# Kernel tuning notes

Hardware: AMD Instinct MI355X
Metric: run time of the kernel (lower is better)

Reference implementation:

```python
import jax, jax.numpy as jnp
import numpy as np

EPS = 1e-5
NUM_HEADS = 8
KEY_DEPTH = 128   # base_filters * key_expansion
VAL_DEPTH = 256   # base_filters * value_expansion
C_IN = 256


def conv1x1(x, w):
    # x: [N, Cin, L], w: [Cout, Cin] (1x1 conv, no bias)
    return jnp.einsum('oc,ncl->nol', w, x)


def group_norm1(x, w, b, eps=EPS):
    # torch GroupNorm(1, C) on [N, C, L]: normalize over (C, L) per sample,
    # per-channel affine.
    mu = jnp.mean(x, axis=(1, 2), keepdims=True)
    var = jnp.var(x, axis=(1, 2), keepdims=True)
    xn = (x - mu) * jax.lax.rsqrt(var + eps)
    return xn * w[None, :, None] + b[None, :, None]


def layer_norm_last2(x, eps=EPS):
    # freshly-constructed nn.LayerNorm([A, B]): weight=1, bias=0 -> pure norm
    mu = jnp.mean(x, axis=(-2, -1), keepdims=True)
    var = jnp.var(x, axis=(-2, -1), keepdims=True)
    return (x - mu) * jax.lax.rsqrt(var + eps)


def gelu(x):
    return jax.nn.gelu(x, approximate=False)  # torch F.gelu default (erf)


def setup_inputs() -> dict:
    key = jax.random.key(0)
    ks = jax.random.split(key, 16)
    N, L = 8, 1024
    qkv_out = 2 * KEY_DEPTH + VAL_DEPTH  # 512

    def w(k, shape, std=0.02):
        return jax.random.normal(k, shape, jnp.float32) * std

    def gw(k, c):
        return 1.0 + 0.1 * jax.random.normal(k, (c,), jnp.float32)

    return {
        'f': jax.random.normal(ks[0], (N, C_IN, L), jnp.float32),
        'w_z': w(ks[1], (C_IN, C_IN), np.sqrt(2.0 / C_IN)),
        'gz_w': gw(ks[2], C_IN), 'gz_b': w(ks[3], (C_IN,)),
        'w_qkv': w(ks[4], (qkv_out, C_IN), C_IN ** -0.5),
        'gq_w': gw(ks[5], qkv_out), 'gq_b': w(ks[6], (qkv_out,)),
        'w_out': w(ks[7], (C_IN, VAL_DEPTH), np.sqrt(2.0 / VAL_DEPTH)),
        'go_w': gw(ks[8], C_IN), 'go_b': w(ks[9], (C_IN,)),
        'w_ffn1': w(ks[10], (2 * C_IN, C_IN), np.sqrt(2.0 / C_IN)),
        'g1_w': gw(ks[11], 2 * C_IN), 'g1_b': w(ks[12], (2 * C_IN,)),
        'w_ffn2': w(ks[13], (C_IN, 2 * C_IN), np.sqrt(1.0 / C_IN)),
        'g2_w': gw(ks[14], C_IN), 'g2_b': w(ks[15], (C_IN,)),
    }


def reference(f, w_z, gz_w, gz_b, w_qkv, gq_w, gq_b, w_out, go_w, go_b,
              w_ffn1, g1_w, g1_b, w_ffn2, g2_w, g2_b):
    N, C, L = f.shape
    H = NUM_HEADS

    z = gelu(group_norm1(conv1x1(gelu(f), w_z), gz_w, gz_b))
    qkv = group_norm1(conv1x1(z, w_qkv), gq_w, gq_b)
    q, k, v = jnp.split(qkv, [KEY_DEPTH, 2 * KEY_DEPTH], axis=1)
    q = q.reshape(N, H, KEY_DEPTH // H, L)
    k = k.reshape(N, H, KEY_DEPTH // H, L)
    v = v.reshape(N, H, VAL_DEPTH // H, L)

    # [N, H, L, L] similarity, no scaling, then LayerNorm over full LxL map
    logits = jnp.einsum('nhcl,nhcm->nhlm', q, k)
    logits = layer_norm_last2(logits)

    # scatter-mask: diagonal -> -inf for every head
    eye = jnp.eye(L, dtype=bool)[None, None]  # [1,1,L,L]
    logits = jnp.where(eye, -jnp.inf, logits)

    attn = jax.nn.softmax(logits.astype(jnp.float32), axis=-1)
    attn = jnp.where(jnp.isnan(attn), 0.0, attn)

    out = jnp.einsum('nhlm,nhdm->nhdl', attn, v).reshape(N, VAL_DEPTH, L)
    out = gelu(layer_norm_last2(out))  # LayerNorm([C_v, L]), fresh params

    out = group_norm1(conv1x1(out, w_out), go_w, go_b)
    f = gelu(f + out)

    h = gelu(group_norm1(conv1x1(f, w_ffn1), g1_w, g1_b))
    h = group_norm1(conv1x1(h, w_ffn2), g2_w, g2_b)
    return gelu(f + h)
```

## Files before the change

### kernel.cpp

```cpp
#include <hip/hip_runtime.h>

#define LSEQ 1024

typedef __attribute__((ext_vector_type(8))) short bf16x8;
typedef __attribute__((ext_vector_type(4))) float f32x4;

__device__ __forceinline__ float gelu_f(float x){
    return 0.5f*x*(1.0f+erff(x*0.7071067811865476f));
}

__device__ __forceinline__ unsigned cvtpk(float lo, float hi){
    unsigned r;
    asm("v_cvt_pk_bf16_f32 %0, %1, %2" : "=v"(r) : "v"(lo), "v"(hi));
    return r;
}

__global__ __launch_bounds__(256,2) void prologue(
    const float* __restrict__ w0, const float* __restrict__ w1,
    const float* __restrict__ w2, const float* __restrict__ w3,
    const float* __restrict__ w4, unsigned short* __restrict__ wdst,
    const float* __restrict__ f, unsigned short* __restrict__ t0,
    float* __restrict__ stats, float* __restrict__ covs)
{
    __shared__ float T[64][68];
    int b = blockIdx.x;
    int tid = threadIdx.x;

    if(b < 512){
        int ltile = (b&15)*64, ctile = ((b>>4)&3)*64, n = b>>6;
        const float* s = f + (size_t)n*256*LSEQ;
        int cl = tid>>4, l4 = (tid&15)*4;
        #pragma unroll
        for(int p=0;p<4;p++){
            int c_loc = p*16 + cl;
            float4 v = *(const float4*)&s[(size_t)(ctile+c_loc)*LSEQ + ltile + l4];
            float4 t;
            t.x = gelu_f(v.x); t.y = gelu_f(v.y); t.z = gelu_f(v.z); t.w = gelu_f(v.w);
            *(float4*)&T[c_loc][l4] = t;
        }
        __syncthreads();
        int l_loc = tid>>2, cg = (tid&3)*16;
        uint4 o0, o1;
        o0.x = cvtpk(T[cg+0][l_loc],  T[cg+1][l_loc]);
        o0.y = cvtpk(T[cg+2][l_loc],  T[cg+3][l_loc]);
        o0.z = cvtpk(T[cg+4][l_loc],  T[cg+5][l_loc]);
        o0.w = cvtpk(T[cg+6][l_loc],  T[cg+7][l_loc]);
        o1.x = cvtpk(T[cg+8][l_loc],  T[cg+9][l_loc]);
        o1.y = cvtpk(T[cg+10][l_loc], T[cg+11][l_loc]);
        o1.z = cvtpk(T[cg+12][l_loc], T[cg+13][l_loc]);
        o1.w = cvtpk(T[cg+14][l_loc], T[cg+15][l_loc]);
        unsigned short* d = t0 + (size_t)n*LSEQ*256 + (size_t)(ltile+l_loc)*256 + ctile + cg;
        *(uint4*)d = o0;
        *(uint4*)(d+8) = o1;
    } else if(b < 1024){
        int idx4 = (b-512)*256 + tid;
        const float* src; int off4;
        if(idx4 < 16384){ src=w0; off4=idx4; }
        else if(idx4 < 49152){ src=w1; off4=idx4-16384; }
        else if(idx4 < 65536){ src=w2; off4=idx4-49152; }
        else if(idx4 < 98304){ src=w3; off4=idx4-65536; }
        else { src=w4; off4=idx4-98304; }
        float4 v = ((const float4*)src)[off4];
        uint2 p; p.x = cvtpk(v.x,v.y); p.y = cvtpk(v.z,v.w);
        ((uint2*)wdst)[idx4] = p;
    } else if(b == 1024){
        if(tid < 64) ((float4*)stats)[tid] = (float4){0.f,0.f,0.f,0.f};
    } else {
        int i = (b-1025)*256 + tid;
        ((float4*)covs)[i] = (float4){0.f,0.f,0.f,0.f};
    }
}

__global__ __launch_bounds__(256,2) void xform_bf16(
    const float* __restrict__ src, const float* __restrict__ res,
    const float* __restrict__ stats,
    const float* __restrict__ gw, const float* __restrict__ gb,
    float cnt_inv, int C, unsigned short* __restrict__ dst)
{
    __shared__ float T[64][68];
    int n = blockIdx.z;
    int ltile = blockIdx.x*64, ctile = blockIdx.y*64;
    int tid = threadIdx.x;

    float mu=0.f, istd=1.f;
    if(stats){
        float s1 = stats[2*n], s2 = stats[2*n+1];
        mu = s1*cnt_inv;
        istd = rsqrtf(s2*cnt_inv - mu*mu + 1e-5f);
    }
    const float* s = src + (size_t)n*C*LSEQ;
    const float* r = res ? res + (size_t)n*C*LSEQ : nullptr;

    int cl = tid>>4, l4 = (tid&15)*4;
    #pragma unroll
    for(int p=0;p<4;p++){
        int c_loc = p*16 + cl;
        int c = ctile + c_loc;
        float w_ = 1.f, b_ = 0.f;
        if(stats){ w_ = istd; b_ = -mu*istd; }
        if(gw){ b_ = gb[c] + b_*gw[c]; w_ *= gw[c]; }
        float4 v = *(const float4*)&s[(size_t)c*LSEQ + ltile + l4];
        float4 t;
        t.x = v.x*w_+b_; t.y = v.y*w_+b_; t.z = v.z*w_+b_; t.w = v.w*w_+b_;
        if(r){
            float4 rv = *(const float4*)&r[(size_t)c*LSEQ + ltile + l4];
            t.x += rv.x; t.y += rv.y; t.z += rv.z; t.w += rv.w;
        }
        t.x = gelu_f(t.x); t.y = gelu_f(t.y); t.z = gelu_f(t.z); t.w = gelu_f(t.w);
        *(float4*)&T[c_loc][l4] = t;
    }
    __syncthreads();

    int l_loc = tid>>2, cg = (tid&3)*16;
    uint4 o0, o1;
    o0.x = cvtpk(T[cg+0][l_loc],  T[cg+1][l_loc]);
    o0.y = cvtpk(T[cg+2][l_loc],  T[cg+3][l_loc]);
    o0.z = cvtpk(T[cg+4][l_loc],  T[cg+5][l_loc]);
    o0.w = cvtpk(T[cg+6][l_loc],  T[cg+7][l_loc]);
    o1.x = cvtpk(T[cg+8][l_loc],  T[cg+9][l_loc]);
    o1.y = cvtpk(T[cg+10][l_loc], T[cg+11][l_loc]);
    o1.z = cvtpk(T[cg+12][l_loc], T[cg+13][l_loc]);
    o1.w = cvtpk(T[cg+14][l_loc], T[cg+15][l_loc]);
    unsigned short* d = dst + (size_t)n*LSEQ*C + (size_t)(ltile+l_loc)*C + ctile + cg;
    *(uint4*)d = o0;
    *(uint4*)(d+8) = o1;
}

__global__ __launch_bounds__(256,2) void gemm_bf16(
    const unsigned short* __restrict__ Abf,
    const unsigned short* __restrict__ Bbf,
    float* __restrict__ C,
    int M, int K,
    float* __restrict__ out_stats)
{
    __shared__ short As[64*264];
    __shared__ short Bs[64*264];

    int tid = threadIdx.x;
    int n = blockIdx.z, n0 = blockIdx.x*64, m0 = blockIdx.y*64;
    int wave = tid>>6, lane = tid&63;
    int col = lane&15, quad = lane>>4;
    int srow = tid>>2, sks = (tid&3)*8;

    const unsigned short* apt = Abf + (size_t)(m0+srow)*K + sks;
    const unsigned short* bpt = Bbf + ((size_t)n*LSEQ + n0+srow)*K + sks;

    f32x4 acc[4];
    #pragma unroll
    for(int t=0;t<4;t++) acc[t] = (f32x4){0.f,0.f,0.f,0.f};

    for(int kp=0; kp<K; kp+=256){
        __syncthreads();
        uint4 av[8], bw[8];
        #pragma unroll
        for(int i=0;i<8;i++) av[i] = *(const uint4*)(apt + kp + i*32);
        #pragma unroll
        for(int i=0;i<8;i++) bw[i] = *(const uint4*)(bpt + kp + i*32);
        #pragma unroll
        for(int i=0;i<8;i++) *(uint4*)&As[srow*264 + sks + i*32] = av[i];
        #pragma unroll
        for(int i=0;i<8;i++) *(uint4*)&Bs[srow*264 + sks + i*32] = bw[i];
        __syncthreads();

        #pragma unroll
        for(int kc=0;kc<8;kc++){
            bf16x8 af = *(bf16x8*)&As[(wave*16+col)*264 + kc*32 + quad*8];
            #pragma unroll
            for(int t=0;t<4;t++){
                bf16x8 bf = *(bf16x8*)&Bs[(t*16+col)*264 + kc*32 + quad*8];
                acc[t] = __builtin_amdgcn_mfma_f32_16x16x32_bf16(af, bf, acc[t], 0,0,0);
            }
        }
    }

    __syncthreads();
    size_t cbase = (size_t)n*M*LSEQ;
    float lsum=0.f, lsq=0.f;
    #pragma unroll
    for(int t=0;t<4;t++){
        #pragma unroll
        for(int r2=0;r2<4;r2++){
            int m = m0 + wave*16 + quad*4 + r2;
            int l = n0 + t*16 + col;
            float v = acc[t][r2];
            C[cbase + (size_t)m*LSEQ + l] = v;
            lsum += v; lsq += v*v;
        }
    }
    float* scr = (float*)As;
    scr[tid] = lsum; scr[256+tid] = lsq;
    __syncthreads();
    for(int s=128;s>0;s>>=1){
        if(tid<s){ scr[tid]+=scr[tid+s]; scr[256+tid]+=scr[256+tid+s]; }
        __syncthreads();
    }
    if(tid==0){
        atomicAdd(&out_stats[2*n],   scr[0]);
        atomicAdd(&out_stats[2*n+1], scr[256]);
    }
}

__global__ __launch_bounds__(256,2) void head_cov(
    const float* __restrict__ qkv,
    const float* __restrict__ s_qkv,
    const float* __restrict__ gq_w, const float* __restrict__ gq_b,
    float* __restrict__ covq, float* __restrict__ covk,
    float* __restrict__ sumq, float* __restrict__ sumk)
{
    __shared__ float Kq[16*132];
    __shared__ float Kk[16*132];
    int b = blockIdx.x;
    int head = b>>3, chunk = b&7;
    int n = head>>3, h = head&7;
    int tid = threadIdx.x;
    int m0 = chunk*128;

    float s1 = s_qkv[2*n], s2v = s_qkv[2*n+1];
    float mu  = s1*(1.f/524288.f);
    float var = s2v*(1.f/524288.f) - mu*mu;
    float istd = rsqrtf(var + 1e-5f);

    const float* base = qkv + (size_t)n*512*LSEQ;
    int m = tid&127, cg = tid>>7;
    #pragma unroll
    for(int cc=0;cc<8;cc++){
        int c = cg*8+cc;
        int chq = h*16+c, chk = 128+h*16+c;
        Kq[c*132+m] = (base[(size_t)chq*LSEQ+m0+m]-mu)*istd*gq_w[chq]+gq_b[chq];
        Kk[c*132+m] = (base[(size_t)chk*LSEQ+m0+m]-mu)*istd*gq_w[chk]+gq_b[chk];
    }
    __syncthreads();

    int i = tid>>4, j = tid&15;
    float q0=0,q1=0,q2=0,q3=0, k0=0,k1=0,k2=0,k3=0;
    for(int mm=0;mm<128;mm+=4){
        float4 qa = *(const float4*)&Kq[i*132+mm];
        float4 qb = *(const float4*)&Kq[j*132+mm];
        q0 += qa.x*qb.x; q1 += qa.y*qb.y; q2 += qa.z*qb.z; q3 += qa.w*qb.w;
        float4 ka = *(const float4*)&Kk[i*132+mm];
        float4 kb = *(const float4*)&Kk[j*132+mm];
        k0 += ka.x*kb.x; k1 += ka.y*kb.y; k2 += ka.z*kb.z; k3 += ka.w*kb.w;
    }
    atomicAdd(&covq[head*256 + i*16 + j], (q0+q1)+(q2+q3));
    atomicAdd(&covk[head*256 + i*16 + j], (k0+k1)+(k2+k3));

    if(i==0){
        float s=0.f;
        for(int mm=0;mm<128;mm+=4){
            float4 v = *(const float4*)&Kq[j*132+mm];
            s += (v.x+v.y)+(v.z+v.w);
        }
        atomicAdd(&sumq[head*16+j], s);
    }
    if(i==1){
        float s=0.f;
        for(int mm=0;mm<128;mm+=4){
            float4 v = *(const float4*)&Kk[j*132+mm];
            s += (v.x+v.y)+(v.z+v.w);
        }
        atomicAdd(&sumk[head*16+j], s);
    }
}

__global__ __launch_bounds__(256) void attn_kernel(
    const float* __restrict__ qkv,
    const float* __restrict__ s_qkv,
    const float* __restrict__ gq_w, const float* __restrict__ gq_b,
    const float* __restrict__ covq, const float* __restrict__ covk,
    const float* __restrict__ sumq, const float* __restrict__ sumk,
    float* __restrict__ out,
    float* __restrict__ out_stats)
{
    __shared__ short Qs[128*40];
    __shared__ short Ks[128*40];
    __shared__ short Vs[32*136];
    __shared__ short Ps[128*152];
    __shared__ float bounds_l[128];
    __shared__ float issum_l[128];
    __shared__ float sred4[4];

    int b = blockIdx.x;
    int head = b&63, rb = b>>6;
    int n = head>>3, h = head&7;
    int tid = threadIdx.x;
    int wv = tid>>6, lane = tid&63;
    int col = lane&15, quad = lane>>4;
    int l0 = rb*128;

    float ih;
    {
        float prod = covq[head*256+tid]*covk[head*256+tid];
        #pragma unroll
        for(int d=1;d<64;d<<=1) prod += __shfl_xor(prod, d);
        if(lane==0) sred4[wv] = prod;
        __syncthreads();
        if(tid==0){
            double S2 = (double)sred4[0] + (double)sred4[1]
                      + (double)sred4[2] + (double)sred4[3];
            double S1 = 0.0;
            for(int c=0;c<16;c++)
                S1 += (double)sumq[head*16+c]*(double)sumk[head*16+c];
            double cnt = 1048576.0;
            double mean = S1/cnt;
            double v2 = S2/cnt - mean*mean;
            if(v2 < 0.0) v2 = 0.0;
            sred4[0] = (float)(1.0/sqrt(v2 + 1e-5));
        }
        __syncthreads();
        ih = sred4[0];
        __syncthreads();
    }
    float ihl = ih * 1.4426950408889634f;

    const float* base = qkv + (size_t)n*512*LSEQ;
    float s1 = s_qkv[2*n], s2v = s_qkv[2*n+1];
    float mu  = s1*(1.f/524288.f);
    float var = s2v*(1.f/524288.f) - mu*mu;
    float istd = rsqrtf(var + 1e-5f);

    {
        int row = tid>>1, hf = tid&1;
        uint4 z = {0,0,0,0};
        *(uint4*)&Qs[row*40 + 16 + hf*8] = z;
        *(uint4*)&Ks[row*40 + 16 + hf*8] = z;
    }

    {
        int row = tid>>1, cg = tid&1;
        float qn2p = 0.f;
        float qv[8];
        #pragma unroll
        for(int cc=0;cc<8;cc++){
            int ch = h*16 + cg*8 + cc;
            float w_ = gq_w[ch]*istd, b_ = gq_b[ch]-mu*istd*gq_w[ch];
            float x = base[(size_t)ch*LSEQ + l0 + row];
            float v = x*w_ + b_;
            qv[cc] = v;
            qn2p += v*v;
        }
        uint4 pq;
        pq.x = cvtpk(qv[0],qv[1]); pq.y = cvtpk(qv[2],qv[3]);
        pq.z = cvtpk(qv[4],qv[5]); pq.w = cvtpk(qv[6],qv[7]);
        *(uint4*)&Qs[row*40 + cg*8] = pq;
        float oth = __shfl_xor(qn2p, 1);
        if(cg==0) bounds_l[row] = sqrtf(qn2p + oth);
    }

    {
        float kn2max = 0.f;
        #pragma unroll
        for(int j=0;j<4;j++){
            int m = tid + j*256;
            float s = 0.f;
            for(int c=0;c<16;c++){
                int ch = 128+h*16+c;
                float x = base[(size_t)ch*LSEQ + m];
                float kv = (x-mu)*istd*gq_w[ch]+gq_b[ch];
                s += kv*kv;
            }
            kn2max = fmaxf(kn2max, s);
        }
        #pragma unroll
        for(int d=1;d<64;d<<=1) kn2max = fmaxf(kn2max, __shfl_xor(kn2max,d));
        if(lane==0) sred4[wv] = kn2max;
    }
    __syncthreads();
    float kmax = sqrtf(fmaxf(fmaxf(sred4[0],sred4[1]),fmaxf(sred4[2],sred4[3])));

    bf16x8 qf[2];
    float B2l[2]; int grow[2];
    #pragma unroll
    for(int t=0;t<2;t++){
        int rl = (2*wv+t)*16 + col;
        qf[t] = *(bf16x8*)&Qs[rl*40 + quad*8];
        B2l[t] = bounds_l[rl]*kmax*ihl;
        grow[t] = l0 + rl;
    }

    int km_l = tid>>1, kg = tid&1;
    float kw8[8], kb8[8];
    #pragma unroll
    for(int cc=0;cc<8;cc++){
        int ch = 128+h*16+kg*8+cc;
        kw8[cc] = gq_w[ch]*istd;
        kb8[cc] = gq_b[ch]-mu*istd*gq_w[ch];
    }
    int vd = tid>>3, vmg = tid&7;
    float vw, vb;
    {
        int ch = 256+h*32+vd;
        vw = gq_w[ch]*istd;
        vb = gq_b[ch]-mu*istd*gq_w[ch];
    }
    const float* kp = base + (size_t)(128+h*16+kg*8)*LSEQ + km_l;
    const float* vp = base + (size_t)(256+h*32+vd)*LSEQ + vmg*16;

    f32x4 acc[2][2];
    #pragma unroll
    for(int t=0;t<2;t++){ acc[t][0]=(f32x4){0,0,0,0}; acc[t][1]=(f32x4){0,0,0,0}; }
    float ssum[2] = {0.f,0.f};
    const f32x4 zero4 = {0.f,0.f,0.f,0.f};

    float kn[8];
    float4 v0n, v1n, v2n, v3n;
    #pragma unroll
    for(int cc=0;cc<8;cc++) kn[cc] = kp[(size_t)cc*LSEQ];
    v0n = *(const float4*)&vp[0];
    v1n = *(const float4*)&vp[4];
    v2n = *(const float4*)&vp[8];
    v3n = *(const float4*)&vp[12];

    for(int mc=0;mc<8;mc++){
        int M0 = mc*128;
        {
            uint4 pk;
            pk.x = cvtpk(kn[0]*kw8[0]+kb8[0], kn[1]*kw8[1]+kb8[1]);
            pk.y = cvtpk(kn[2]*kw8[2]+kb8[2], kn[3]*kw8[3]+kb8[3]);
            pk.z = cvtpk(kn[4]*kw8[4]+kb8[4], kn[5]*kw8[5]+kb8[5]);
            pk.w = cvtpk(kn[6]*kw8[6]+kb8[6], kn[7]*kw8[7]+kb8[7]);
            *(uint4*)&Ks[km_l*40 + kg*8] = pk;
        }
        {
            uint4 p0, p1;
            p0.x = cvtpk(v0n.x*vw+vb, v0n.y*vw+vb);
            p0.y = cvtpk(v0n.z*vw+vb, v0n.w*vw+vb);
            p0.z = cvtpk(v1n.x*vw+vb, v1n.y*vw+vb);
            p0.w = cvtpk(v1n.z*vw+vb, v1n.w*vw+vb);
            p1.x = cvtpk(v2n.x*vw+vb, v2n.y*vw+vb);
            p1.y = cvtpk(v2n.z*vw+vb, v2n.w*vw+vb);
            p1.z = cvtpk(v3n.x*vw+vb, v3n.y*vw+vb);
            p1.w = cvtpk(v3n.z*vw+vb, v3n.w*vw+vb);
            *(uint4*)&Vs[vd*136 + vmg*16]     = p0;
            *(uint4*)&Vs[vd*136 + vmg*16 + 8] = p1;
        }
        __syncthreads();

        if(mc < 7){
            int M1 = M0 + 128;
            #pragma unroll
            for(int cc=0;cc<8;cc++) kn[cc] = kp[(size_t)cc*LSEQ + M1];
            v0n = *(const float4*)&vp[M1];
            v1n = *(const float4*)&vp[M1+4];
            v2n = *(const float4*)&vp[M1+8];
            v3n = *(const float4*)&vp[M1+12];
        }

        __builtin_amdgcn_s_setprio(1);
        bool diag_mc = (mc == rb);
        #pragma unroll
        for(int mt=0;mt<8;mt++){
            bf16x8 ak = *(bf16x8*)&Ks[(mt*16+col)*40 + quad*8];
            #pragma unroll
            for(int t=0;t<2;t++){
                f32x4 sc = __builtin_amdgcn_mfma_f32_16x16x32_bf16(ak, qf[t], zero4, 0,0,0);
                float pr[4];
                #pragma unroll
                for(int r=0;r<4;r++)
                    pr[r] = exp2f(fmaf(sc[r], ihl, -B2l[t]));
                if(diag_mc){
                    int mbase = M0 + mt*16 + quad*4;
                    #pragma unroll
                    for(int r=0;r<4;r++)
                        if(mbase + r == grow[t]) pr[r] = 0.f;
                }
                ssum[t] += (pr[0]+pr[1])+(pr[2]+pr[3]);
                uint2 pw;
                pw.x = cvtpk(pr[0],pr[1]); pw.y = cvtpk(pr[2],pr[3]);
                *(uint2*)&Ps[((2*wv+t)*16+col)*152 + mt*16 + quad*4] = pw;
            }
        }
        #pragma unroll
        for(int kk=0;kk<4;kk++){
            bf16x8 bv0 = *(bf16x8*)&Vs[( col)*136 + kk*32 + quad*8];
            bf16x8 bv1 = *(bf16x8*)&Vs[((16+col))*136 + kk*32 + quad*8];
            #pragma unroll
            for(int t=0;t<2;t++){
                bf16x8 ap = *(bf16x8*)&Ps[((2*wv+t)*16+col)*152 + kk*32 + quad*8];
                acc[t][0] = __builtin_amdgcn_mfma_f32_16x16x32_bf16(ap, bv0, acc[t][0], 0,0,0);
                acc[t][1] = __builtin_amdgcn_mfma_f32_16x16x32_bf16(ap, bv1, acc[t][1], 0,0,0);
            }
        }
        __builtin_amdgcn_s_setprio(0);
        __syncthreads();
    }

    #pragma unroll
    for(int t=0;t<2;t++){
        float v = ssum[t];
        v += __shfl_xor(v,16);
        v += __shfl_xor(v,32);
        if(quad==0) issum_l[(2*wv+t)*16+col] = v;
    }
    __syncthreads();
    if(tid<128) issum_l[tid] = 1.f/issum_l[tid];
    __syncthreads();

    float* ep = (float*)Ps;
    #pragma unroll
    for(int t=0;t<2;t++)
        #pragma unroll
        for(int dt=0;dt<2;dt++)
            *(f32x4*)&ep[(dt*16+col)*132 + (2*wv+t)*16 + quad*4] = acc[t][dt];
    __syncthreads();

    float lsum=0.f, lsq=0.f;
    size_t obase = (size_t)n*262144 + (size_t)h*32*LSEQ + l0;
    #pragma unroll
    for(int t=0;t<16;t++){
        int idx = t*256 + tid;
        int d = idx>>7, row = idx&127;
        float y = ep[d*132+row]*issum_l[row];
        out[obase + (size_t)d*LSEQ + row] = y;
        lsum += y; lsq += y*y;
    }
    float* red = (float*)Ks;
    red[tid]=lsum; red[256+tid]=lsq;
    __syncthreads();
    for(int s=128;s>0;s>>=1){
        if(tid<s){ red[tid]+=red[tid+s]; red[256+tid]+=red[256+tid+s]; }
        __syncthreads();
    }
    if(tid==0){
        atomicAdd(&out_stats[2*n],   red[0]);
        atomicAdd(&out_stats[2*n+1], red[256]);
    }
}

__global__ __launch_bounds__(256) void ew_final(
    const float* __restrict__ f, const float* __restrict__ x,
    const float* __restrict__ h2,
    const float* __restrict__ sx, const float* __restrict__ sh,
    const float* __restrict__ go_w, const float* __restrict__ go_b,
    const float* __restrict__ g2_w, const float* __restrict__ g2_b,
    float* __restrict__ out)
{
    int idx = blockIdx.x*256 + threadIdx.x;
    int n = idx >> 16;
    int c = (idx >> 8) & 255;
    float mux, isx, muh, ish;
    {
        float s1 = sx[2*n], s2 = sx[2*n+1];
        mux = s1*(1.f/262144.f);
        isx = rsqrtf(s2*(1.f/262144.f) - mux*mux + 1e-5f);
        float t1 = sh[2*n], t2 = sh[2*n+1];
        muh = t1*(1.f/262144.f);
        ish = rsqrtf(t2*(1.f/262144.f) - muh*muh + 1e-5f);
    }
    float wo = go_w[c]*isx, bo = go_b[c]-mux*isx*go_w[c];
    float w2 = g2_w[c]*ish, b2 = g2_b[c]-muh*ish*g2_w[c];
    float4 xv = ((const float4*)x)[idx];
    float4 fv = ((const float4*)f)[idx];
    float4 hv = ((const float4*)h2)[idx];
    float4 ov;
    float f1;
    f1 = gelu_f(fv.x + xv.x*wo+bo); ov.x = gelu_f(f1 + hv.x*w2+b2);
    f1 = gelu_f(fv.y + xv.y*wo+bo); ov.y = gelu_f(f1 + hv.y*w2+b2);
    f1 = gelu_f(fv.z + xv.z*wo+bo); ov.z = gelu_f(f1 + hv.z*w2+b2);
    f1 = gelu_f(fv.w + xv.w*wo+bo); ov.w = gelu_f(f1 + hv.w*w2+b2);
    ((float4*)out)[idx] = ov;
}

extern "C" void kernel_launch(void* const* d_in, const int* in_sizes, int n_in,
                              void* d_out, int out_size, void* d_ws, size_t ws_size,
                              hipStream_t stream) {
    const float* f     = (const float*)d_in[0];
    const float* w_z   = (const float*)d_in[1];
    const float* gz_w  = (const float*)d_in[2];
    const float* gz_b  = (const float*)d_in[3];
    const float* w_qkv = (const float*)d_in[4];
    const float* gq_w  = (const float*)d_in[5];
    const float* gq_b  = (const float*)d_in[6];
    const float* w_out = (const float*)d_in[7];
    const float* go_w  = (const float*)d_in[8];
    const float* go_b  = (const float*)d_in[9];
    const float* w_f1  = (const float*)d_in[10];
    const float* g1_w  = (const float*)d_in[11];
    const float* g1_b  = (const float*)d_in[12];
    const float* w_f2  = (const float*)d_in[13];
    const float* g2_w  = (const float*)d_in[14];
    const float* g2_b  = (const float*)d_in[15];

    float* ws = (float*)d_ws;
    float* stats = ws;
    float* s_z    = stats + 0;
    float* s_qkv  = stats + 16;
    float* s_attn = stats + 32;
    float* s_x    = stats + 48;
    float* s_h1   = stats + 64;
    float* s_h2   = stats + 80;

    float* qkvF = ws + 256;
    float* z0F  = qkvF + 4194304;
    float* xF   = z0F + 2097152;
    unsigned short* t0 = (unsigned short*)(xF + 2097152);
    unsigned short* t1 = t0 + 2097152;
    unsigned short* wp = t1 + 2097152;
    unsigned short* t4 = (unsigned short*)z0F;
    unsigned short* wp_z   = wp;
    unsigned short* wp_qkv = wp + 65536;
    unsigned short* wp_out = wp + 196608;
    unsigned short* wp_f1  = wp + 262144;
    unsigned short* wp_f2  = wp + 393216;

    float* covq = xF;
    float* covk = xF + 16384;
    float* sumq = xF + 32768;
    float* sumk = xF + 33792;

    float* outp = (float*)d_out;

    dim3 blk(256);
    prologue<<<1059,blk,0,stream>>>(w_z, w_qkv, w_out, w_f1, w_f2, wp,
        f, t0, stats, covq);
    gemm_bf16<<<dim3(16,4,8),blk,0,stream>>>(wp_z, t0, z0F, 256, 256, s_z);
    xform_bf16<<<dim3(16,4,8),blk,0,stream>>>(z0F, nullptr, s_z, gz_w, gz_b,
        1.f/262144.f, 256, t1);
    gemm_bf16<<<dim3(16,8,8),blk,0,stream>>>(wp_qkv, t1, qkvF, 512, 256, s_qkv);
    head_cov<<<512,blk,0,stream>>>(qkvF, s_qkv, gq_w, gq_b, covq, covk, sumq, sumk);
    attn_kernel<<<512,blk,0,stream>>>(qkvF, s_qkv, gq_w, gq_b,
        covq, covk, sumq, sumk, z0F, s_attn);
    xform_bf16<<<dim3(16,4,8),blk,0,stream>>>(z0F, nullptr, s_attn, nullptr, nullptr,
        1.f/262144.f, 256, t0);
    gemm_bf16<<<dim3(16,4,8),blk,0,stream>>>(wp_out, t0, xF, 256, 256, s_x);
    xform_bf16<<<dim3(16,4,8),blk,0,stream>>>(xF, f, s_x, go_w, go_b,
        1.f/262144.f, 256, t1);
    gemm_bf16<<<dim3(16,8,8),blk,0,stream>>>(wp_f1, t1, qkvF, 512, 256, s_h1);
    xform_bf16<<<dim3(16,8,8),blk,0,stream>>>(qkvF, nullptr, s_h1, g1_w, g1_b,
        1.f/524288.f, 512, t4);
    gemm_bf16<<<dim3(16,4,8),blk,0,stream>>>(wp_f2, t4, qkvF, 256, 512, s_h2);
    ew_final<<<2048,blk,0,stream>>>(f, xF, qkvF, s_x, s_h2,
        go_w, go_b, g2_w, g2_b, outp);
}
```

Before: 298.2 us.

## Precompute bf16 Q/K/V and norms in head_cov; halve attention row tile

head_cov now normalizes Q, K and V once, writes them as packed bf16 in attention-friendly layouts, and records per-row q norms and a per-head max k norm via atomicMax. Before this, every attention block re-read fp32 qkv, redid the GroupNorm affine and rescanned all keys for the k-norm bound. The attention kernel now just copies the bf16 tiles into LDS. It also moves from 128 to 64 query rows per block with one MFMA row tile per wave, so the grid doubles to 1024 blocks for more parallelism. In exchange each K/V tile is reused by fewer query rows, head_cov writes more data, and workspace buffers are aliased.

Measured after the change: 312.2 us. +4.7%, slower.

```diff
diff --git a/kernel.cpp b/kernel.cpp
--- a/kernel.cpp
+++ b/kernel.cpp
@@ -20,7 +20,8 @@
     const float* __restrict__ w2, const float* __restrict__ w3,
     const float* __restrict__ w4, unsigned short* __restrict__ wdst,
     const float* __restrict__ f, unsigned short* __restrict__ t0,
-    float* __restrict__ stats, float* __restrict__ covs)
+    float* __restrict__ stats, float* __restrict__ covs,
+    unsigned* __restrict__ kmaxu)
 {
     __shared__ float T[64][68];
     int b = blockIdx.x;
@@ -65,6 +66,7 @@
         ((uint2*)wdst)[idx4] = p;
     } else if(b == 1024){
         if(tid < 64) ((float4*)stats)[tid] = (float4){0.f,0.f,0.f,0.f};
+        if(tid >= 64 && tid < 80) ((uint4*)kmaxu)[tid-64] = (uint4){0,0,0,0};
     } else {
         int i = (b-1025)*256 + tid;
         ((float4*)covs)[i] = (float4){0.f,0.f,0.f,0.f};
@@ -205,7 +207,10 @@
     const float* __restrict__ s_qkv,
     const float* __restrict__ gq_w, const float* __restrict__ gq_b,
     float* __restrict__ covq, float* __restrict__ covk,
-    float* __restrict__ sumq, float* __restrict__ sumk)
+    float* __restrict__ sumq, float* __restrict__ sumk,
+    unsigned short* __restrict__ Qbf, unsigned short* __restrict__ Kbf,
+    unsigned short* __restrict__ Vbf,
+    float* __restrict__ qnorm, unsigned* __restrict__ kmaxu)
 {
     __shared__ float Kq[16*132];
     __shared__ float Kk[16*132];
@@ -228,6 +233,29 @@
         int chq = h*16+c, chk = 128+h*16+c;
         Kq[c*132+m] = (base[(size_t)chq*LSEQ+m0+m]-mu)*istd*gq_w[chq]+gq_b[chq];
         Kk[c*132+m] = (base[(size_t)chk*LSEQ+m0+m]-mu)*istd*gq_w[chk]+gq_b[chk];
+    }
+
+    {
+        int d = tid>>3, mg = tid&7;
+        int ch = 256 + h*32 + d;
+        float vw = gq_w[ch]*istd, vb = gq_b[ch]-mu*istd*gq_w[ch];
+        const float* vs = base + (size_t)ch*LSEQ + m0 + mg*16;
+        float4 a0 = *(const float4*)&vs[0];
+        float4 a1 = *(const float4*)&vs[4];
+        float4 a2 = *(const float4*)&vs[8];
+        float4 a3 = *(const float4*)&vs[12];
+        uint4 p0, p1;
+        p0.x = cvtpk(a0.x*vw+vb, a0.y*vw+vb);
+        p0.y = cvtpk(a0.z*vw+vb, a0.w*vw+vb);
+        p0.z = cvtpk(a1.x*vw+vb, a1.y*vw+vb);
+        p0.w = cvtpk(a1.z*vw+vb, a1.w*vw+vb);
+        p1.x = cvtpk(a2.x*vw+vb, a2.y*vw+vb);
+        p1.y = cvtpk(a2.z*vw+vb, a2.w*vw+vb);
+        p1.z = cvtpk(a3.x*vw+vb, a3.y*vw+vb);
+        p1.w = cvtpk(a3.z*vw+vb, a3.w*vw+vb);
+        unsigned short* dv = Vbf + ((size_t)head*32 + d)*1024 + m0 + mg*16;
+        *(uint4*)dv = p0;
+        *(uint4*)(dv+8) = p1;
     }
     __syncthreads();
 
@@ -260,23 +288,55 @@
         }
         atomicAdd(&sumk[head*16+j], s);
     }
+
+    {
+        int mm2 = tid & 127;
+        if(tid < 128){
+            unsigned u[8]; float s2 = 0.f;
+            #pragma unroll
+            for(int c=0;c<16;c+=2){
+                float a = Kq[c*132+mm2], b2 = Kq[(c+1)*132+mm2];
+                s2 += a*a + b2*b2;
+                u[c>>1] = cvtpk(a, b2);
+            }
+            unsigned short* dq = Qbf + ((size_t)head*1024 + m0 + mm2)*16;
+            *(uint4*)dq     = *(uint4*)&u[0];
+            *(uint4*)(dq+8) = *(uint4*)&u[4];
+            qnorm[head*1024 + m0 + mm2] = s2;
+        } else {
+            unsigned u[8]; float s2 = 0.f;
+            #pragma unroll
+            for(int c=0;c<16;c+=2){
+                float a = Kk[c*132+mm2], b2 = Kk[(c+1)*132+mm2];
+                s2 += a*a + b2*b2;
+                u[c>>1] = cvtpk(a, b2);
+            }
+            unsigned short* dk = Kbf + ((size_t)head*1024 + m0 + mm2)*16;
+            *(uint4*)dk     = *(uint4*)&u[0];
+            *(uint4*)(dk+8) = *(uint4*)&u[4];
+            #pragma unroll
+            for(int d=1;d<64;d<<=1) s2 = fmaxf(s2, __shfl_xor(s2, d));
+            if((tid&63)==0) atomicMax(kmaxu + head, __float_as_uint(s2));
+        }
+    }
 }
 
 __global__ __launch_bounds__(256) void attn_kernel(
-    const float* __restrict__ qkv,
-    const float* __restrict__ s_qkv,
-    const float* __restrict__ gq_w, const float* __restrict__ gq_b,
+    const unsigned short* __restrict__ Qbf,
+    const unsigned short* __restrict__ Kbf,
+    const unsigned short* __restrict__ Vbf,
+    const float* __restrict__ qnorm, const unsigned* __restrict__ kmaxu,
     const float* __restrict__ covq, const float* __restrict__ covk,
     const float* __restrict__ sumq, const float* __restrict__ sumk,
     float* __restrict__ out,
     float* __restrict__ out_stats)
 {
-    __shared__ short Qs[128*40];
+    __shared__ short Qs[64*40];
     __shared__ short Ks[128*40];
     __shared__ short Vs[32*136];
-    __shared__ short Ps[128*152];
-    __shared__ float bounds_l[128];
-    __shared__ float issum_l[128];
+    __shared__ short Ps[64*152];
+    __shared__ float bounds_l[64];
+    __shared__ float issum_l[64];
     __shared__ float sred4[4];
 
     int b = blockIdx.x;
@@ -285,7 +345,7 @@
     int tid = threadIdx.x;
     int wv = tid>>6, lane = tid&63;
     int col = lane&15, quad = lane>>4;
-    int l0 = rb*128;
+    int l0 = rb*64;
 
     float ih;
     {
@@ -308,208 +368,113 @@
         }
         __syncthreads();
         ih = sred4[0];
-        __syncthreads();
     }
     float ihl = ih * 1.4426950408889634f;
 
-    const float* base = qkv + (size_t)n*512*LSEQ;
-    float s1 = s_qkv[2*n], s2v = s_qkv[2*n+1];
-    float mu  = s1*(1.f/524288.f);
-    float var = s2v*(1.f/524288.f) - mu*mu;
-    float istd = rsqrtf(var + 1e-5f);
-
     {
+        uint4 z = {0,0,0,0};
         int row = tid>>1, hf = tid&1;
-        uint4 z = {0,0,0,0};
-        *(uint4*)&Qs[row*40 + 16 + hf*8] = z;
         *(uint4*)&Ks[row*40 + 16 + hf*8] = z;
-    }
-
-    {
-        int row = tid>>1, cg = tid&1;
-        float qn2p = 0.f;
-        float qv[8];
-        #pragma unroll
-        for(int cc=0;cc<8;cc++){
-            int ch = h*16 + cg*8 + cc;
-            float w_ = gq_w[ch]*istd, b_ = gq_b[ch]-mu*istd*gq_w[ch];
-            float x = base[(size_t)ch*LSEQ + l0 + row];
-            float v = x*w_ + b_;
-            qv[cc] = v;
-            qn2p += v*v;
-        }
-        uint4 pq;
-        pq.x = cvtpk(qv[0],qv[1]); pq.y = cvtpk(qv[2],qv[3]);
-        pq.z = cvtpk(qv[4],qv[5]); pq.w = cvtpk(qv[6],qv[7]);
-        *(uint4*)&Qs[row*40 + cg*8] = pq;
-        float oth = __shfl_xor(qn2p, 1);
-        if(cg==0) bounds_l[row] = sqrtf(qn2p + oth);
-    }
-
-    {
-        float kn2max = 0.f;
-        #pragma unroll
-        for(int j=0;j<4;j++){
-            int m = tid + j*256;
-            float s = 0.f;
-            for(int c=0;c<16;c++){
-                int ch = 128+h*16+c;
-                float x = base[(size_t)ch*LSEQ + m];
-                float kv = (x-mu)*istd*gq_w[ch]+gq_b[ch];
-                s += kv*kv;
-            }
-            kn2max = fmaxf(kn2max, s);
-        }
-        #pragma unroll
-        for(int d=1;d<64;d<<=1) kn2max = fmaxf(kn2max, __shfl_xor(kn2max,d));
-        if(lane==0) sred4[wv] = kn2max;
-    }
-    __syncthreads();
-    float kmax = sqrtf(fmaxf(fmaxf(sred4[0],sred4[1]),fmaxf(sred4[2],sred4[3])));
-
-    bf16x8 qf[2];
-    float B2l[2]; int grow[2];
-    #pragma unroll
-    for(int t=0;t<2;t++){
-        int rl = (2*wv+t)*16 + col;
-        qf[t] = *(bf16x8*)&Qs[rl*40 + quad*8];
-        B2l[t] = bounds_l[rl]*kmax*ihl;
-        grow[t] = l0 + rl;
-    }
-
-    int km_l = tid>>1, kg = tid&1;
-    float kw8[8], kb8[8];
-    #pragma unroll
-    for(int cc=0;cc<8;cc++){
-        int ch = 128+h*16+kg*8+cc;
-        kw8[cc] = gq_w[ch]*istd;
-        kb8[cc] = gq_b[ch]-mu*istd*gq_w[ch];
-    }
-    int vd = tid>>3, vmg = tid&7;
-    float vw, vb;
-    {
-        int ch = 256+h*32+vd;
-        vw = gq_w[ch]*istd;
-        vb = gq_b[ch]-mu*istd*gq_w[ch];
-    }
-    const float* kp = base + (size_t)(128+h*16+kg*8)*LSEQ + km_l;
-    const float* vp = base + (size_t)(256+h*32+vd)*LSEQ + vmg*16;
-
-    f32x4 acc[2][2];
-    #pragma unroll
-    for(int t=0;t<2;t++){ acc[t][0]=(f32x4){0,0,0,0}; acc[t][1]=(f32x4){0,0,0,0}; }
-    float ssum[2] = {0.f,0.f};
+        if(row < 64) *(uint4*)&Qs[row*40 + 16 + hf*8] = z;
+        if(tid < 64){
+            const unsigned short* qsrc = Qbf + ((size_t)head*1024 + l0 + tid)*16;
+            *(uint4*)&Qs[tid*40]     = *(const uint4*)qsrc;
+            *(uint4*)&Qs[tid*40 + 8] = *(const uint4*)(qsrc + 8);
+            bounds_l[tid] = sqrtf(qnorm[head*1024 + l0 + tid]);
+        }
+    }
+    float kmax = sqrtf(__uint_as_float(kmaxu[head]));
+    __syncthreads();
+
+    int rl = wv*16 + col;
+    bf16x8 qf = *(bf16x8*)&Qs[rl*40 + quad*8];
+    float B2l = bounds_l[rl]*kmax*ihl;
+    int grow = l0 + rl;
+
+    int krow = tid>>1, khalf = tid&1;
+    const unsigned short* ksrc = Kbf + ((size_t)head*1024 + krow)*16 + khalf*8;
+    int vdd = tid>>3, vmg = tid&7;
+    const unsigned short* vsrc = Vbf + ((size_t)head*32 + vdd)*1024 + vmg*16;
+
+    f32x4 acc[2];
+    acc[0]=(f32x4){0,0,0,0}; acc[1]=(f32x4){0,0,0,0};
+    float ssum = 0.f;
     const f32x4 zero4 = {0.f,0.f,0.f,0.f};
 
-    float kn[8];
-    float4 v0n, v1n, v2n, v3n;
-    #pragma unroll
-    for(int cc=0;cc<8;cc++) kn[cc] = kp[(size_t)cc*LSEQ];
-    v0n = *(const float4*)&vp[0];
-    v1n = *(const float4*)&vp[4];
-    v2n = *(const float4*)&vp[8];
-    v3n = *(const float4*)&vp[12];
-
+    uint4 kreg = *(const uint4*)ksrc;
+    uint4 vr0  = *(const uint4*)vsrc;
+    uint4 vr1  = *(const uint4*)(vsrc + 8);
+
+    int diag_mc = rb>>1;
     for(int mc=0;mc<8;mc++){
         int M0 = mc*128;
-        {
-            uint4 pk;
-            pk.x = cvtpk(kn[0]*kw8[0]+kb8[0], kn[1]*kw8[1]+kb8[1]);
-            pk.y = cvtpk(kn[2]*kw8[2]+kb8[2], kn[3]*kw8[3]+kb8[3]);
-            pk.z = cvtpk(kn[4]*kw8[4]+kb8[4], kn[5]*kw8[5]+kb8[5]);
-            pk.w = cvtpk(kn[6]*kw8[6]+kb8[6], kn[7]*kw8[7]+kb8[7]);
-            *(uint4*)&Ks[km_l*40 + kg*8] = pk;
-        }
-        {
-            uint4 p0, p1;
-            p0.x = cvtpk(v0n.x*vw+vb, v0n.y*vw+vb);
-            p0.y = cvtpk(v0n.z*vw+vb, v0n.w*vw+vb);
-            p0.z = cvtpk(v1n.x*vw+vb, v1n.y*vw+vb);
-            p0.w = cvtpk(v1n.z*vw+vb, v1n.w*vw+vb);
-            p1.x = cvtpk(v2n.x*vw+vb, v2n.y*vw+vb);
-            p1.y = cvtpk(v2n.z*vw+vb, v2n.w*vw+vb);
-            p1.z = cvtpk(v3n.x*vw+vb, v3n.y*vw+vb);
-            p1.w = cvtpk(v3n.z*vw+vb, v3n.w*vw+vb);
-            *(uint4*)&Vs[vd*136 + vmg*16]     = p0;
-            *(uint4*)&Vs[vd*136 + vmg*16 + 8] = p1;
-        }
+        *(uint4*)&Ks[krow*40 + khalf*8]  = kreg;
+        *(uint4*)&Vs[vdd*136 + vmg*16]     = vr0;
+        *(uint4*)&Vs[vdd*136 + vmg*16 + 8] = vr1;
         __syncthreads();
 
         if(mc < 7){
-            int M1 = M0 + 128;
-            #pragma unroll
-            for(int cc=0;cc<8;cc++) kn[cc] = kp[(size_t)cc*LSEQ + M1];
-            v0n = *(const float4*)&vp[M1];
-            v1n = *(const float4*)&vp[M1+4];
-            v2n = *(const float4*)&vp[M1+8];
-            v3n = *(const float4*)&vp[M1+12];
+            kreg = *(const uint4*)(ksrc + (size_t)(M0+128)*16);
+            vr0  = *(const uint4*)(vsrc + M0+128);
+            vr1  = *(const uint4*)(vsrc + M0+136);
         }
 
         __builtin_amdgcn_s_setprio(1);
-        bool diag_mc = (mc == rb);
+        bool dg = (mc == diag_mc);
         #pragma unroll
         for(int mt=0;mt<8;mt++){
             bf16x8 ak = *(bf16x8*)&Ks[(mt*16+col)*40 + quad*8];
+            f32x4 sc = __builtin_amdgcn_mfma_f32_16x16x32_bf16(ak, qf, zero4, 0,0,0);
+            float pr[4];
             #pragma unroll
-            for(int t=0;t<2;t++){
-                f32x4 sc = __builtin_amdgcn_mfma_f32_16x16x32_bf16(ak, qf[t], zero4, 0,0,0);
-                float pr[4];
+            for(int r=0;r<4;r++)
+                pr[r] = exp2f(fmaf(sc[r], ihl, -B2l));
+            if(dg){
+                int mbase = M0 + mt*16 + quad*4;
                 #pragma unroll
                 for(int r=0;r<4;r++)
-                    pr[r] = exp2f(fmaf(sc[r], ihl, -B2l[t]));
-                if(diag_mc){
-                    int mbase = M0 + mt*16 + quad*4;
-                    #pragma unroll
-                    for(int r=0;r<4;r++)
-                        if(mbase + r == grow[t]) pr[r] = 0.f;
-                }
-                ssum[t] += (pr[0]+pr[1])+(pr[2]+pr[3]);
-                uint2 pw;
-                pw.x = cvtpk(pr[0],pr[1]); pw.y = cvtpk(pr[2],pr[3]);
-                *(uint2*)&Ps[((2*wv+t)*16+col)*152 + mt*16 + quad*4] = pw;
+                    if(mbase + r == grow) pr[r] = 0.f;
             }
+            ssum += (pr[0]+pr[1])+(pr[2]+pr[3]);
+            uint2 pw;
+            pw.x = cvtpk(pr[0],pr[1]); pw.y = cvtpk(pr[2],pr[3]);
+            *(uint2*)&Ps[rl*152 + mt*16 + quad*4] = pw;
         }
         #pragma unroll
         for(int kk=0;kk<4;kk++){
             bf16x8 bv0 = *(bf16x8*)&Vs[( col)*136 + kk*32 + quad*8];
-            bf16x8 bv1 = *(bf16x8*)&Vs[((16+col))*136 + kk*32 + quad*8];
-            #pragma unroll
-            for(int t=0;t<2;t++){
-                bf16x8 ap = *(bf16x8*)&Ps[((2*wv+t)*16+col)*152 + kk*32 + quad*8];
-                acc[t][0] = __builtin_amdgcn_mfma_f32_16x16x32_bf16(ap, bv0, acc[t][0], 0,0,0);
-                acc[t][1] = __builtin_amdgcn_mfma_f32_16x16x32_bf16(ap, bv1, acc[t][1], 0,0,0);
-            }
+            bf16x8 bv1 = *(bf16x8*)&Vs[(16+col)*136 + kk*32 + quad*8];
+            bf16x8 ap = *(bf16x8*)&Ps[rl*152 + kk*32 + quad*8];
+            acc[0] = __builtin_amdgcn_mfma_f32_16x16x32_bf16(ap, bv0, acc[0], 0,0,0);
+            acc[1] = __builtin_amdgcn_mfma_f32_16x16x32_bf16(ap, bv1, acc[1], 0,0,0);
         }
         __builtin_amdgcn_s_setprio(0);
         __syncthreads();
     }
 
-    #pragma unroll
-    for(int t=0;t<2;t++){
-        float v = ssum[t];
+    {
+        float v = ssum;
         v += __shfl_xor(v,16);
         v += __shfl_xor(v,32);
-        if(quad==0) issum_l[(2*wv+t)*16+col] = v;
-    }
-    __syncthreads();
-    if(tid<128) issum_l[tid] = 1.f/issum_l[tid];
+        if(quad==0) issum_l[rl] = v;
+    }
+    __syncthreads();
+    if(tid<64) issum_l[tid] = 1.f/issum_l[tid];
     __syncthreads();
 
     float* ep = (float*)Ps;
     #pragma unroll
-    for(int t=0;t<2;t++)
-        #pragma unroll
-        for(int dt=0;dt<2;dt++)
-            *(f32x4*)&ep[(dt*16+col)*132 + (2*wv+t)*16 + quad*4] = acc[t][dt];
+    for(int dt=0;dt<2;dt++)
+        *(f32x4*)&ep[(dt*16+col)*68 + wv*16 + quad*4] = acc[dt];
     __syncthreads();
 
     float lsum=0.f, lsq=0.f;
     size_t obase = (size_t)n*262144 + (size_t)h*32*LSEQ + l0;
     #pragma unroll
-    for(int t=0;t<16;t++){
+    for(int t=0;t<8;t++){
         int idx = t*256 + tid;
-        int d = idx>>7, row = idx&127;
-        float y = ep[d*132+row]*issum_l[row];
+        int d = idx>>6, row = idx&63;
+        float y = ep[d*68+row]*issum_l[row];
         out[obase + (size_t)d*LSEQ + row] = y;
         lsum += y; lsq += y*y;
     }
@@ -606,18 +571,25 @@
     float* covk = xF + 16384;
     float* sumq = xF + 32768;
     float* sumk = xF + 33792;
+    float* qnorm = xF + 34816;
+    unsigned* kmaxu = (unsigned*)(xF + 100352);
+
+    unsigned short* Qbf = t0;
+    unsigned short* Kbf = t0 + 1048576;
+    unsigned short* Vbf = t1;
 
     float* outp = (float*)d_out;
 
     dim3 blk(256);
     prologue<<<1059,blk,0,stream>>>(w_z, w_qkv, w_out, w_f1, w_f2, wp,
-        f, t0, stats, covq);
+        f, t0, stats, covq, kmaxu);
     gemm_bf16<<<dim3(16,4,8),blk,0,stream>>>(wp_z, t0, z0F, 256, 256, s_z);
     xform_bf16<<<dim3(16,4,8),blk,0,stream>>>(z0F, nullptr, s_z, gz_w, gz_b,
         1.f/262144.f, 256, t1);
     gemm_bf16<<<dim3(16,8,8),blk,0,stream>>>(wp_qkv, t1, qkvF, 512, 256, s_qkv);
-    head_cov<<<512,blk,0,stream>>>(qkvF, s_qkv, gq_w, gq_b, covq, covk, sumq, sumk);
-    attn_kernel<<<512,blk,0,stream>>>(qkvF, s_qkv, gq_w, gq_b,
+    head_cov<<<512,blk,0,stream>>>(qkvF, s_qkv, gq_w, gq_b, covq, covk, sumq, sumk,
+        Qbf, Kbf, Vbf, qnorm, kmaxu);
+    attn_kernel<<<1024,blk,0,stream>>>(Qbf, Kbf, Vbf, qnorm, kmaxu,
         covq, covk, sumq, sumk, z0F, s_attn);
     xform_bf16<<<dim3(16,4,8),blk,0,stream>>>(z0F, nullptr, s_attn, nullptr, nullptr,
         1.f/262144.f, 256, t0);
```
